# Performance work log

Hardware: AMD Instinct MI355X
Metric: run time of the kernel (lower is better)

Reference implementation:

```python
import jax, jax.numpy as jnp
import numpy as np
from math import sqrt

B, TS_D, SEG, D, H = 16, 2, 1024, 256, 8
D_FF = 1024
DK = D // H
EPS = 1e-5


def _layernorm(x, g, b):
    mu = jnp.mean(x, axis=-1, keepdims=True)
    var = jnp.mean(jnp.square(x - mu), axis=-1, keepdims=True)
    return (x - mu) * jax.lax.rsqrt(var + EPS) * g + b


def setup_inputs() -> dict:
    key = jax.random.key(0)
    ks = jax.random.split(key, 16)
    s = 0.02
    return {
        "x": jax.random.normal(ks[0], (B, TS_D, SEG, D), dtype=jnp.float32),
        "Wq": jax.random.normal(ks[1], (D, D), dtype=jnp.float32) * s,
        "bq": jnp.zeros((D,), jnp.float32),
        "Wk": jax.random.normal(ks[2], (D, D), dtype=jnp.float32) * s,
        "bk": jnp.zeros((D,), jnp.float32),
        "Wv": jax.random.normal(ks[3], (D, D), dtype=jnp.float32) * s,
        "bv": jnp.zeros((D,), jnp.float32),
        "Wo": jax.random.normal(ks[4], (D, D), dtype=jnp.float32) * s,
        "bo": jnp.zeros((D,), jnp.float32),
        "g31": jnp.ones((D,), jnp.float32),
        "b31": jnp.zeros((D,), jnp.float32),
        "W1": jax.random.normal(ks[5], (D, D_FF), dtype=jnp.float32) * s,
        "b1": jnp.zeros((D_FF,), jnp.float32),
        "W2": jax.random.normal(ks[6], (D_FF, D), dtype=jnp.float32) * s,
        "b2": jnp.zeros((D,), jnp.float32),
        "g41": jnp.ones((D,), jnp.float32),
        "b41": jnp.zeros((D,), jnp.float32),
    }


def reference(x, Wq, bq, Wk, bk, Wv, bv, Wo, bo, g31, b31, W1, b1, W2, b2, g41, b41):
    # x: [B, ts_d=2, seg, d]; output is final_out2 (only live path of the module)
    b, ts_d, seg, d = x.shape
    scale = 1.0 / sqrt(DK)
    segments = x.reshape(b, ts_d * seg, d)            # [B, 2*seg, d]
    Q = (segments @ Wq + bq).reshape(b, -1, H, DK)
    K = (segments @ Wk + bk).reshape(b, -1, H, DK)
    V = (segments @ Wv + bv).reshape(b, -1, H, DK)
    q = Q[:, :seg]       # first seg positions (channel 0)
    k = K[:, -seg:]      # last seg positions (channel 1)
    v = V[:, -seg:]
    # cross-segment dual attention
    A1 = jax.nn.softmax(scale * jnp.einsum('blhe,bshe->bhls', q, k), axis=-1)
    out1 = jnp.einsum('bhls,bshd->blhd', A1, v).reshape(b, seg, d)
    A2 = jax.nn.softmax(scale * jnp.einsum('blhe,bshe->bhls', k, q), axis=-1)
    out2 = jnp.einsum('bhls,bshd->blhd', A2, q).reshape(b, seg, d)
    y = jnp.concatenate([out1, out2], axis=1) @ Wo + bo   # [B, 2*seg, d]
    h = _layernorm(segments + y, g31, b31)
    mlp = jax.nn.gelu(h @ W1 + b1, approximate=False) @ W2 + b2
    h = _layernorm(h + mlp, g41, b41)
    return h.reshape(b, ts_d, seg, d)
```

## Files before the change

### kernel.cpp

```cpp
#include <hip/hip_runtime.h>
#include <hip/hip_bf16.h>
#include <math.h>

#define BATCH 16
#define SEG 1024
#define DMODEL 256
#define NH 8
#define DK 32
#define DFF 1024
#define NTOK (BATCH * 2 * SEG)
#define EPS 1e-5f

typedef __attribute__((ext_vector_type(8))) short short8;
typedef __attribute__((ext_vector_type(4))) short short4b;
typedef __attribute__((ext_vector_type(4))) float f32x4;

#if __has_builtin(__builtin_amdgcn_exp2f)
#define EXP2(x) __builtin_amdgcn_exp2f(x)
#else
#define EXP2(x) __expf((x) * 0.6931471805599453f)
#endif

__device__ __forceinline__ ushort f2bf(float x) {
    union { float f; unsigned u; } a; a.f = x;
    unsigned r = a.u + 0x7fffu + ((a.u >> 16) & 1u);
    return (ushort)(r >> 16);
}

typedef const __attribute__((address_space(1))) unsigned gas_u32;
typedef __attribute__((address_space(3))) unsigned las_u32;
__device__ __forceinline__ void gload_lds16(const ushort* g, ushort* l) {
    __builtin_amdgcn_global_load_lds((gas_u32*)g, (las_u32*)l, 16, 0, 0);
}

__global__ __launch_bounds__(256) void wfrag_kernel(
    const float* __restrict__ src, ushort* __restrict__ dst, int K, int N, int order)
{
    const int tid = blockIdx.x * 256 + threadIdx.x;
    const int KT_ = K >> 5, NT_ = N >> 4;
    const int total = KT_ * NT_ * 64;
    if (tid >= total) return;
    const int lane = tid & 63;
    const int frag = tid >> 6;
    int kt, nt;
    if (order) { kt = frag / NT_; nt = frag % NT_; }
    else       { nt = frag / KT_; kt = frag % KT_; }
    const int quad = lane >> 4, l = lane & 15;
    const float* s = src + (size_t)(kt * 32 + quad * 8) * N + nt * 16 + l;
    short8 v;
#pragma unroll
    for (int j = 0; j < 8; j++) v[j] = (short)f2bf(s[(size_t)j * N]);
    *(short8*)&dst[(size_t)tid * 8] = v;
}

#define ASTR 264

__device__ __forceinline__ void dense256_pass(
    const ushort* __restrict__ Wf, ushort* WL, const short8* af,
    f32x4* acc, int t, int w, int lane)
{
#pragma unroll
    for (int nt = 0; nt < 16; ++nt) acc[nt] = (f32x4){0.f, 0.f, 0.f, 0.f};
    {
        const ushort* g = Wf + (size_t)w * 4096 + lane * 8;
        ushort* ld = WL + w * 4096;
#pragma unroll
        for (int i = 0; i < 8; ++i) gload_lds16(g + i * 512, ld + i * 512);
    }
    __syncthreads();
    for (int c = 0; c < 4; ++c) {
        if (c < 3) {
            const ushort* g = Wf + (size_t)(c + 1) * 16384 + w * 4096 + lane * 8;
            ushort* ld = WL + ((c + 1) & 1) * 8192 + w * 4096;
#pragma unroll
            for (int i = 0; i < 8; ++i) gload_lds16(g + i * 512, ld + i * 512);
        }
        const ushort* buf = WL + (c & 1) * 8192;
#pragma unroll
        for (int n2 = 0; n2 < 4; ++n2)
#pragma unroll
            for (int kt = 0; kt < 8; ++kt) {
                const short8 bf_ = *(const short8*)&buf[(n2 * 8 + kt) * 512 + lane * 8];
                acc[c * 4 + n2] = __builtin_amdgcn_mfma_f32_16x16x32_bf16(af[kt], bf_, acc[c * 4 + n2], 0, 0, 0);
            }
        __syncthreads();
    }
}

__global__ __launch_bounds__(256) void qkv_mfma_kernel(
    const float* __restrict__ x,
    const ushort* __restrict__ Wqf, const float* __restrict__ bq,
    const ushort* __restrict__ Wkf, const float* __restrict__ bk,
    const ushort* __restrict__ Wvf, const float* __restrict__ bv,
    ushort* __restrict__ qbuf, ushort* __restrict__ kbuf,
    ushort* __restrict__ qt, ushort* __restrict__ vt)
{
    __shared__ __align__(16) ushort SM[64 * ASTR];
    const int bid = blockIdx.x;
    const int which = bid >> 8;
    const int sub = bid & 255;
    const int b = sub >> 4, ti = sub & 15;
    const int half = (which == 0) ? 0 : 1;
    const int t = threadIdx.x;
    const int w = t >> 6, lane = t & 63, l = lane & 15, quad = lane >> 4;

    const float* xrow = x + ((size_t)b * 2048 + (size_t)half * 1024 + ti * 64) * 256;
#pragma unroll
    for (int p = 0; p < 16; ++p) {
        int ch = t + 256 * p;
        int row = ch >> 6, c4 = ch & 63;
        float4 v = *(const float4*)&xrow[row * 256 + c4 * 4];
        uint2 pk;
        pk.x = (unsigned)f2bf(v.x) | ((unsigned)f2bf(v.y) << 16);
        pk.y = (unsigned)f2bf(v.z) | ((unsigned)f2bf(v.w) << 16);
        *(uint2*)&SM[row * ASTR + c4 * 4] = pk;
    }
    __syncthreads();

    short8 af[8];
#pragma unroll
    for (int kt = 0; kt < 8; ++kt)
        af[kt] = *(const short8*)&SM[(w * 16 + l) * ASTR + kt * 32 + quad * 8];
    __syncthreads();

    const ushort* Wf  = (which == 0) ? Wqf : (which == 1 ? Wkf : Wvf);
    const float* bias = (which == 0) ? bq  : (which == 1 ? bk  : bv);
    const float kscale = (which == 1) ? 0.25503472f : 1.0f;

    f32x4 acc[16];
    dense256_pass(Wf, SM, af, acc, t, w, lane);

    ushort bfv[16][4];
#pragma unroll
    for (int nt = 0; nt < 16; ++nt) {
        const float bb = bias[nt * 16 + l];
#pragma unroll
        for (int r = 0; r < 4; ++r) bfv[nt][r] = f2bf((acc[nt][r] + bb) * kscale);
    }

    if (which <= 1) {
        ushort* obuf = which ? kbuf : qbuf;
#pragma unroll
        for (int nt = 0; nt < 16; ++nt) {
            const int h = nt >> 1, e = (nt & 1) * 16 + l;
#pragma unroll
            for (int r = 0; r < 4; ++r) {
                int tok = ti * 64 + w * 16 + quad * 4 + r;
                obuf[(((size_t)b * 8 + h) * SEG + tok) * 32 + e] = bfv[nt][r];
            }
        }
    }
    if (which != 1) {
        ushort* tb = which ? vt : qt;
#pragma unroll
        for (int nt = 0; nt < 16; ++nt)
#pragma unroll
            for (int r = 0; r < 4; ++r)
                SM[(nt * 16 + l) * 66 + w * 16 + quad * 4 + r] = bfv[nt][r];
        __syncthreads();
        const int d = t, hh = t >> 5, e = t & 31;
        ushort* dr = tb + (((size_t)b * 8 + hh) * 32 + e) * 1024 + ti * 64;
#pragma unroll
        for (int j = 0; j < 8; ++j) {
            uint2 v;
            v.x = *(const unsigned*)&SM[d * 66 + j * 8];
            v.y = *(const unsigned*)&SM[d * 66 + j * 8 + 2];
            unsigned z0 = *(const unsigned*)&SM[d * 66 + j * 8 + 4];
            unsigned z1 = *(const unsigned*)&SM[d * 66 + j * 8 + 6];
            *(uint4*)&dr[j * 8] = make_uint4(v.x, v.y, z0, z1);
        }
    }
}

#define KTILE 128
#define KP 40
#define VP 132

__global__ __launch_bounds__(256) void attn_mfma_kernel(
    const ushort* __restrict__ qbuf, const ushort* __restrict__ kbuf,
    const ushort* __restrict__ qt, const ushort* __restrict__ vt,
    ushort* __restrict__ abuf)
{
    __shared__ __align__(16) ushort Kl[KTILE * KP];
    __shared__ __align__(16) ushort Vl[32 * VP];

    const int bid   = blockIdx.x;
    const int sbh   = bid & 255;
    const int qtile = bid >> 8;
    const int stage = sbh >> 7;
    const int b     = (sbh >> 3) & 15;
    const int h     = sbh & 7;

    const ushort* Qm = stage ? kbuf : qbuf;
    const ushort* Km = stage ? qbuf : kbuf;
    const ushort* Vt = stage ? qt : vt;
    const size_t bh = ((size_t)b * 8 + h) * SEG * 32;

    const int t    = threadIdx.x;
    const int w    = t >> 6;
    const int lane = t & 63;
    const int l    = lane & 15;
    const int quad = lane >> 4;

    const int qrow = qtile * 64 + w * 16 + l;
    const short8 qf = *(const short8*)&Qm[bh + (size_t)qrow * 32 + quad * 8];

    f32x4 o0 = {0.f, 0.f, 0.f, 0.f};
    f32x4 o1 = {0.f, 0.f, 0.f, 0.f};
    f32x4 o2 = {0.f, 0.f, 0.f, 0.f};
    const short4b ones = {(short)0x3F80, (short)0x3F80, (short)0x3F80, (short)0x3F80};

    for (int tile = 0; tile < 8; ++tile) {
        __syncthreads();
        const ushort* Kg = &Km[bh + (size_t)(tile * KTILE) * 32];
#pragma unroll
        for (int p = 0; p < 2; ++p) {
            int ch = t + 256 * p;
            int row = ch >> 2, part = ch & 3;
            *(short8*)&Kl[row * KP + part * 8] = *(const short8*)&Kg[row * 32 + part * 8];
        }
        const ushort* Vg = &Vt[bh + (size_t)tile * KTILE];
#pragma unroll
        for (int p = 0; p < 2; ++p) {
            int ch = t + 256 * p;
            int d = ch >> 4, c = ch & 15;
            *(short8*)&Vl[d * VP + c * 8] = *(const short8*)&Vg[(size_t)d * 1024 + c * 8];
        }
        __syncthreads();

#pragma unroll
        for (int kb = 0; kb < 8; ++kb) {
            const short8 kf = *(const short8*)&Kl[(kb * 16 + l) * KP + quad * 8];
            f32x4 z = {0.f, 0.f, 0.f, 0.f};
            f32x4 sc = __builtin_amdgcn_mfma_f32_16x16x32_bf16(kf, qf, z, 0, 0, 0);
            union { float f; unsigned u; } a0, a1, a2, a3;
            a0.f = EXP2(sc[0]); a1.f = EXP2(sc[1]);
            a2.f = EXP2(sc[2]); a3.f = EXP2(sc[3]);
            unsigned lo = __builtin_amdgcn_perm(a1.u, a0.u, 0x07060302u);
            unsigned hi = __builtin_amdgcn_perm(a3.u, a2.u, 0x07060302u);
            union { uint2 u; short4b s; } pk; pk.u = make_uint2(lo, hi);
            const short4b vf0 = *(const short4b*)&Vl[l * VP + kb * 16 + quad * 4];
            const short4b vf1 = *(const short4b*)&Vl[(16 + l) * VP + kb * 16 + quad * 4];
            o0 = __builtin_amdgcn_mfma_f32_16x16x16bf16_1k(vf0, pk.s, o0, 0, 0, 0);
            o1 = __builtin_amdgcn_mfma_f32_16x16x16bf16_1k(vf1, pk.s, o1, 0, 0, 0);
            o2 = __builtin_amdgcn_mfma_f32_16x16x16bf16_1k(ones, pk.s, o2, 0, 0, 0);
        }
    }

    const float inv = 1.0f / o2[0];
#pragma unroll
    for (int r = 0; r < 4; ++r) { o0[r] *= inv; o1[r] *= inv; }

    __syncthreads();
    ushort* Ob = &Kl[w * 16 * 40];
#pragma unroll
    for (int r = 0; r < 4; ++r) {
        Ob[l * 40 + quad * 4 + r]      = f2bf(o0[r]);
        Ob[l * 40 + 16 + quad * 4 + r] = f2bf(o1[r]);
    }
    __syncthreads();
    const int q = lane >> 2, part = lane & 3;
    const short8 ov = *(const short8*)&Ob[q * 40 + part * 8];
    const int tok = qtile * 64 + w * 16 + q;
    *(short8*)&abuf[((size_t)b * 2 * SEG + (size_t)stage * SEG + tok) * 256 + h * 32 + part * 8] = ov;
}

__global__ __launch_bounds__(256) void proj_mfma_kernel(
    const ushort* __restrict__ abuf, const ushort* __restrict__ Wof,
    const float* __restrict__ bo, const float* __restrict__ x,
    const float* __restrict__ g31, const float* __restrict__ b31,
    float* __restrict__ hout)
{
    __shared__ __align__(16) ushort SM[64 * ASTR];
    const int bid = blockIdx.x;
    const size_t tok0 = (size_t)bid * 64;
    const int t = threadIdx.x;
    const int w = t >> 6, lane = t & 63, l = lane & 15, quad = lane >> 4;

#pragma unroll
    for (int p = 0; p < 8; ++p) {
        int ch = t + 256 * p;
        int row = ch >> 5, c8 = ch & 31;
        *(short8*)&SM[row * ASTR + c8 * 8] = *(const short8*)&abuf[(tok0 + row) * 256 + c8 * 8];
    }
    __syncthreads();

    short8 af[8];
#pragma unroll
    for (int kt = 0; kt < 8; ++kt)
        af[kt] = *(const short8*)&SM[(w * 16 + l) * ASTR + kt * 32 + quad * 8];
    __syncthreads();

    f32x4 acc[16];
    dense256_pass(Wof, SM, af, acc, t, w, lane);

#pragma unroll
    for (int nt = 0; nt < 16; ++nt) {
        const int d = nt * 16 + l;
        const float bv = bo[d];
#pragma unroll
        for (int r = 0; r < 4; ++r) {
            size_t tok = tok0 + w * 16 + quad * 4 + r;
            acc[nt][r] += bv + x[tok * 256 + d];
        }
    }

    float mu_[4], is_[4];
#pragma unroll
    for (int r = 0; r < 4; ++r) {
        float s = 0.f;
#pragma unroll
        for (int nt = 0; nt < 16; ++nt) s += acc[nt][r];
        s += __shfl_xor(s, 1); s += __shfl_xor(s, 2);
        s += __shfl_xor(s, 4); s += __shfl_xor(s, 8);
        float mu = s * (1.0f / 256.0f);
        float vs = 0.f;
#pragma unroll
        for (int nt = 0; nt < 16; ++nt) { float dd = acc[nt][r] - mu; vs += dd * dd; }
        vs += __shfl_xor(vs, 1); vs += __shfl_xor(vs, 2);
        vs += __shfl_xor(vs, 4); vs += __shfl_xor(vs, 8);
        mu_[r] = mu;
        is_[r] = rsqrtf(vs * (1.0f / 256.0f) + EPS);
    }

#pragma unroll
    for (int nt = 0; nt < 16; ++nt) {
        const int d = nt * 16 + l;
        const float gg = g31[d], bb = b31[d];
#pragma unroll
        for (int r = 0; r < 4; ++r) {
            size_t tok = tok0 + w * 16 + quad * 4 + r;
            hout[tok * 256 + d] = (acc[nt][r] - mu_[r]) * is_[r] * gg + bb;
        }
    }
}

#define GP 40

__global__ __launch_bounds__(256) void mlp_mfma_kernel(
    const float* __restrict__ W1dummy_unused, const ushort* __restrict__ W1f,
    const float* __restrict__ b1, const ushort* __restrict__ W2f,
    const float* __restrict__ b2, const float* __restrict__ g41,
    const float* __restrict__ b41, float* __restrict__ io)
{
    __shared__ __align__(16) ushort SM[2 * 16384];
    __shared__ __align__(16) ushort G[4][16 * GP];
    __shared__ __align__(16) float B1L[DFF];
    const int bid = blockIdx.x;
    const size_t tok0 = (size_t)bid * 64;
    const int t = threadIdx.x;
    const int w = t >> 6, lane = t & 63, l = lane & 15, quad = lane >> 4;

    const float* hrow = io + tok0 * 256;
#pragma unroll
    for (int p = 0; p < 16; ++p) {
        int ch = t + 256 * p;
        int row = ch >> 6, c4 = ch & 63;
        float4 v = *(const float4*)&hrow[row * 256 + c4 * 4];
        uint2 pk;
        pk.x = (unsigned)f2bf(v.x) | ((unsigned)f2bf(v.y) << 16);
        pk.y = (unsigned)f2bf(v.z) | ((unsigned)f2bf(v.w) << 16);
        *(uint2*)&SM[row * ASTR + c4 * 4] = pk;
    }
    *(float4*)&B1L[t * 4] = *(const float4*)&b1[t * 4];
    __syncthreads();

    short8 af[8];
#pragma unroll
    for (int kt = 0; kt < 8; ++kt)
        af[kt] = *(const short8*)&SM[(w * 16 + l) * ASTR + kt * 32 + quad * 8];
    __syncthreads();

    f32x4 out[16];
#pragma unroll
    for (int nt = 0; nt < 16; ++nt) out[nt] = (f32x4){0.f, 0.f, 0.f, 0.f};

    ushort* Gw = &G[w][0];

    {
        const ushort* g1 = W1f + w * 2048 + lane * 8;
        const ushort* g2 = W2f + w * 2048 + lane * 8;
        ushort* l1 = SM + w * 2048;
        ushort* l2 = SM + 8192 + w * 2048;
#pragma unroll
        for (int i = 0; i < 4; ++i) {
            gload_lds16(g1 + i * 512, l1 + i * 512);
            gload_lds16(g2 + i * 512, l2 + i * 512);
        }
    }
    __syncthreads();

    for (int c = 0; c < 32; ++c) {
        if (c < 31) {
            const int nb = (c + 1) & 1;
            const ushort* g1 = W1f + (size_t)(c + 1) * 8192 + w * 2048 + lane * 8;
            ushort* l1 = SM + nb * 16384 + w * 2048;
            const ushort* g2 = W2f + (size_t)(c + 1) * 8192 + w * 2048 + lane * 8;
            ushort* l2 = SM + nb * 16384 + 8192 + w * 2048;
#pragma unroll
            for (int i = 0; i < 4; ++i) {
                gload_lds16(g1 + i * 512, l1 + i * 512);
                gload_lds16(g2 + i * 512, l2 + i * 512);
            }
        }
        const ushort* WL = SM + (c & 1) * 16384;

        f32x4 s[2];
        s[0] = (f32x4){0.f, 0.f, 0.f, 0.f};
        s[1] = (f32x4){0.f, 0.f, 0.f, 0.f};
#pragma unroll
        for (int n2 = 0; n2 < 2; ++n2)
#pragma unroll
            for (int kt = 0; kt < 8; ++kt) {
                const short8 bf_ = *(const short8*)&WL[(n2 * 8 + kt) * 512 + lane * 8];
                s[n2] = __builtin_amdgcn_mfma_f32_16x16x32_bf16(af[kt], bf_, s[n2], 0, 0, 0);
            }

#pragma unroll
        for (int n2 = 0; n2 < 2; ++n2) {
            const float bv = B1L[c * 32 + n2 * 16 + l];
#pragma unroll
            for (int r = 0; r < 4; ++r) {
                float v = s[n2][r] + bv;
                float au = fabsf(v) * 0.70710678118654752f;
                float t1 = __builtin_amdgcn_rcpf(fmaf(0.3275911f, au, 1.0f));
                float e  = EXP2(au * au * -1.4426950408889634f);
                float p5 = fmaf(fmaf(fmaf(fmaf(1.061405429f, t1, -1.453152027f),
                                t1, 1.421413741f), t1, -0.284496736f), t1, 0.254829592f) * t1;
                float erf_abs = fmaf(-p5, e, 1.0f);
                float gl = fmaf(0.5f * fabsf(v), erf_abs, 0.5f * v);
                Gw[(quad * 4 + r) * GP + n2 * 16 + l] = f2bf(gl);
            }
        }

        const short8 gf = *(const short8*)&Gw[l * GP + quad * 8];
#pragma unroll
        for (int nt = 0; nt < 16; ++nt) {
            const short8 bf_ = *(const short8*)&WL[8192 + nt * 512 + lane * 8];
            out[nt] = __builtin_amdgcn_mfma_f32_16x16x32_bf16(gf, bf_, out[nt], 0, 0, 0);
        }
        __syncthreads();
    }

#pragma unroll
    for (int nt = 0; nt < 16; ++nt) {
        const int d = nt * 16 + l;
        const float bv = b2[d];
#pragma unroll
        for (int r = 0; r < 4; ++r) {
            size_t tok = tok0 + w * 16 + quad * 4 + r;
            out[nt][r] += bv + io[tok * 256 + d];
        }
    }

    float mu_[4], is_[4];
#pragma unroll
    for (int r = 0; r < 4; ++r) {
        float s = 0.f;
#pragma unroll
        for (int nt = 0; nt < 16; ++nt) s += out[nt][r];
        s += __shfl_xor(s, 1); s += __shfl_xor(s, 2);
        s += __shfl_xor(s, 4); s += __shfl_xor(s, 8);
        float mu = s * (1.0f / 256.0f);
        float vs = 0.f;
#pragma unroll
        for (int nt = 0; nt < 16; ++nt) { float dd = out[nt][r] - mu; vs += dd * dd; }
        vs += __shfl_xor(vs, 1); vs += __shfl_xor(vs, 2);
        vs += __shfl_xor(vs, 4); vs += __shfl_xor(vs, 8);
        mu_[r] = mu;
        is_[r] = rsqrtf(vs * (1.0f / 256.0f) + EPS);
    }

#pragma unroll
    for (int nt = 0; nt < 16; ++nt) {
        const int d = nt * 16 + l;
        const float gg = g41[d], bb = b41[d];
#pragma unroll
        for (int r = 0; r < 4; ++r) {
            size_t tok = tok0 + w * 16 + quad * 4 + r;
            io[tok * 256 + d] = (out[nt][r] - mu_[r]) * is_[r] * gg + bb;
        }
    }
}

extern "C" void kernel_launch(void* const* d_in, const int* in_sizes, int n_in,
                              void* d_out, int out_size, void* d_ws, size_t ws_size,
                              hipStream_t stream)
{
    const float* x   = (const float*)d_in[0];
    const float* Wq  = (const float*)d_in[1];
    const float* bq  = (const float*)d_in[2];
    const float* Wk  = (const float*)d_in[3];
    const float* bk  = (const float*)d_in[4];
    const float* Wv  = (const float*)d_in[5];
    const float* bv  = (const float*)d_in[6];
    const float* Wo  = (const float*)d_in[7];
    const float* bo  = (const float*)d_in[8];
    const float* g31 = (const float*)d_in[9];
    const float* b31 = (const float*)d_in[10];
    const float* W1  = (const float*)d_in[11];
    const float* b1  = (const float*)d_in[12];
    const float* W2  = (const float*)d_in[13];
    const float* b2  = (const float*)d_in[14];
    const float* g41 = (const float*)d_in[15];
    const float* b41 = (const float*)d_in[16];

    float* out = (float*)d_out;

    const size_t HALF = (size_t)BATCH * SEG * DMODEL;
    ushort* qbuf = (ushort*)d_ws;
    ushort* kbuf = qbuf + HALF;
    ushort* qt   = kbuf + HALF;
    ushort* vt   = qt + HALF;
    ushort* abuf = vt + HALF;
    ushort* Wqf  = abuf + 2 * HALF;
    ushort* Wkf  = Wqf + 65536;
    ushort* Wvf  = Wkf + 65536;
    ushort* Wof  = Wvf + 65536;
    ushort* W1f  = Wof + 65536;
    ushort* W2f  = W1f + 262144;

    wfrag_kernel<<<32, 256, 0, stream>>>(Wq, Wqf, 256, 256, 0);
    wfrag_kernel<<<32, 256, 0, stream>>>(Wk, Wkf, 256, 256, 0);
    wfrag_kernel<<<32, 256, 0, stream>>>(Wv, Wvf, 256, 256, 0);
    wfrag_kernel<<<32, 256, 0, stream>>>(Wo, Wof, 256, 256, 0);
    wfrag_kernel<<<128, 256, 0, stream>>>(W1, W1f, 256, 1024, 0);
    wfrag_kernel<<<128, 256, 0, stream>>>(W2, W2f, 1024, 256, 1);

    qkv_mfma_kernel<<<768, 256, 0, stream>>>(x, Wqf, bq, Wkf, bk, Wvf, bv,
                                             qbuf, kbuf, qt, vt);
    attn_mfma_kernel<<<2 * BATCH * NH * (SEG / 64), 256, 0, stream>>>(qbuf, kbuf, qt, vt, abuf);
    proj_mfma_kernel<<<NTOK / 64, 256, 0, stream>>>(abuf, Wof, bo, x, g31, b31, out);
    mlp_mfma_kernel<<<NTOK / 64, 256, 0, stream>>>(nullptr, W1f, b1, W2f, b2, g41, b41, out);
}
```

Before: 284.9 us.

## Fuse projection and MLP kernels, batch weight conversion, prefetch K/V tiles

Merges the six weight-fragment conversion launches into one kernel that picks its matrix by block index. Fuses the output-projection plus LayerNorm kernel into the MLP kernel, so h stays in registers and LDS as bf16 instead of going through global memory in fp32. The attention kernel now register-prefetches the next K/V tile while the current one is computed, with a different K row mapping. The fused kernel keeps more live registers (acc plus out), and the __launch_bounds__(256,2) hint may force register spilling.

```diff
diff --git a/kernel.cpp b/kernel.cpp
--- a/kernel.cpp
+++ b/kernel.cpp
@@ -33,13 +33,24 @@
     __builtin_amdgcn_global_load_lds((gas_u32*)g, (las_u32*)l, 16, 0, 0);
 }
 
-__global__ __launch_bounds__(256) void wfrag_kernel(
-    const float* __restrict__ src, ushort* __restrict__ dst, int K, int N, int order)
+__global__ __launch_bounds__(256) void wfrag_all_kernel(
+    const float* __restrict__ Wq, const float* __restrict__ Wk,
+    const float* __restrict__ Wv, const float* __restrict__ Wo,
+    const float* __restrict__ W1, const float* __restrict__ W2,
+    ushort* __restrict__ Wqf, ushort* __restrict__ Wkf,
+    ushort* __restrict__ Wvf, ushort* __restrict__ Wof,
+    ushort* __restrict__ W1f, ushort* __restrict__ W2f)
 {
-    const int tid = blockIdx.x * 256 + threadIdx.x;
+    const int blk = blockIdx.x;
+    const float* src; ushort* dst; int K, N, order, base;
+    if (blk < 32)       { src = Wq; dst = Wqf; K = 256;  N = 256;  order = 0; base = 0;   }
+    else if (blk < 64)  { src = Wk; dst = Wkf; K = 256;  N = 256;  order = 0; base = 32;  }
+    else if (blk < 96)  { src = Wv; dst = Wvf; K = 256;  N = 256;  order = 0; base = 64;  }
+    else if (blk < 128) { src = Wo; dst = Wof; K = 256;  N = 256;  order = 0; base = 96;  }
+    else if (blk < 256) { src = W1; dst = W1f; K = 256;  N = 1024; order = 0; base = 128; }
+    else                { src = W2; dst = W2f; K = 1024; N = 256;  order = 1; base = 256; }
+    const int tid = (blk - base) * 256 + threadIdx.x;
     const int KT_ = K >> 5, NT_ = N >> 4;
-    const int total = KT_ * NT_ * 64;
-    if (tid >= total) return;
     const int lane = tid & 63;
     const int frag = tid >> 6;
     int kt, nt;
@@ -210,23 +221,35 @@
     f32x4 o2 = {0.f, 0.f, 0.f, 0.f};
     const short4b ones = {(short)0x3F80, (short)0x3F80, (short)0x3F80, (short)0x3F80};
 
+    const int ch0 = t, ch1 = t + 256;
+    const int kr0 = ((ch0 >> 6) << 4) | (ch0 & 15), kp0 = (ch0 >> 4) & 3;
+    const int kr1 = ((ch1 >> 6) << 4) | (ch1 & 15), kp1 = (ch1 >> 4) & 3;
+    const int vd0 = ch0 >> 4, vc0 = ch0 & 15;
+    const int vd1 = ch1 >> 4, vc1 = ch1 & 15;
+    const ushort* Kgb = &Km[bh];
+    const ushort* Vgb = &Vt[bh];
+
+    short8 rk0 = *(const short8*)&Kgb[(size_t)kr0 * 32 + kp0 * 8];
+    short8 rk1 = *(const short8*)&Kgb[(size_t)kr1 * 32 + kp1 * 8];
+    short8 rv0 = *(const short8*)&Vgb[(size_t)vd0 * 1024 + vc0 * 8];
+    short8 rv1 = *(const short8*)&Vgb[(size_t)vd1 * 1024 + vc1 * 8];
+
     for (int tile = 0; tile < 8; ++tile) {
         __syncthreads();
-        const ushort* Kg = &Km[bh + (size_t)(tile * KTILE) * 32];
-#pragma unroll
-        for (int p = 0; p < 2; ++p) {
-            int ch = t + 256 * p;
-            int row = ch >> 2, part = ch & 3;
-            *(short8*)&Kl[row * KP + part * 8] = *(const short8*)&Kg[row * 32 + part * 8];
-        }
-        const ushort* Vg = &Vt[bh + (size_t)tile * KTILE];
-#pragma unroll
-        for (int p = 0; p < 2; ++p) {
-            int ch = t + 256 * p;
-            int d = ch >> 4, c = ch & 15;
-            *(short8*)&Vl[d * VP + c * 8] = *(const short8*)&Vg[(size_t)d * 1024 + c * 8];
-        }
+        *(short8*)&Kl[kr0 * KP + kp0 * 8] = rk0;
+        *(short8*)&Kl[kr1 * KP + kp1 * 8] = rk1;
+        *(short8*)&Vl[vd0 * VP + vc0 * 8] = rv0;
+        *(short8*)&Vl[vd1 * VP + vc1 * 8] = rv1;
         __syncthreads();
+
+        if (tile < 7) {
+            const size_t ko = (size_t)(tile + 1) * KTILE * 32;
+            const size_t vo = (size_t)(tile + 1) * KTILE;
+            rk0 = *(const short8*)&Kgb[ko + (size_t)kr0 * 32 + kp0 * 8];
+            rk1 = *(const short8*)&Kgb[ko + (size_t)kr1 * 32 + kp1 * 8];
+            rv0 = *(const short8*)&Vgb[vo + (size_t)vd0 * 1024 + vc0 * 8];
+            rv1 = *(const short8*)&Vgb[vo + (size_t)vd1 * 1024 + vc1 * 8];
+        }
 
 #pragma unroll
         for (int kb = 0; kb < 8; ++kb) {
@@ -265,83 +288,16 @@
     *(short8*)&abuf[((size_t)b * 2 * SEG + (size_t)stage * SEG + tok) * 256 + h * 32 + part * 8] = ov;
 }
 
-__global__ __launch_bounds__(256) void proj_mfma_kernel(
+#define GP 40
+
+__global__ __launch_bounds__(256, 2) void proj_mlp_kernel(
     const ushort* __restrict__ abuf, const ushort* __restrict__ Wof,
     const float* __restrict__ bo, const float* __restrict__ x,
     const float* __restrict__ g31, const float* __restrict__ b31,
-    float* __restrict__ hout)
-{
-    __shared__ __align__(16) ushort SM[64 * ASTR];
-    const int bid = blockIdx.x;
-    const size_t tok0 = (size_t)bid * 64;
-    const int t = threadIdx.x;
-    const int w = t >> 6, lane = t & 63, l = lane & 15, quad = lane >> 4;
-
-#pragma unroll
-    for (int p = 0; p < 8; ++p) {
-        int ch = t + 256 * p;
-        int row = ch >> 5, c8 = ch & 31;
-        *(short8*)&SM[row * ASTR + c8 * 8] = *(const short8*)&abuf[(tok0 + row) * 256 + c8 * 8];
-    }
-    __syncthreads();
-
-    short8 af[8];
-#pragma unroll
-    for (int kt = 0; kt < 8; ++kt)
-        af[kt] = *(const short8*)&SM[(w * 16 + l) * ASTR + kt * 32 + quad * 8];
-    __syncthreads();
-
-    f32x4 acc[16];
-    dense256_pass(Wof, SM, af, acc, t, w, lane);
-
-#pragma unroll
-    for (int nt = 0; nt < 16; ++nt) {
-        const int d = nt * 16 + l;
-        const float bv = bo[d];
-#pragma unroll
-        for (int r = 0; r < 4; ++r) {
-            size_t tok = tok0 + w * 16 + quad * 4 + r;
-            acc[nt][r] += bv + x[tok * 256 + d];
-        }
-    }
-
-    float mu_[4], is_[4];
-#pragma unroll
-    for (int r = 0; r < 4; ++r) {
-        float s = 0.f;
-#pragma unroll
-        for (int nt = 0; nt < 16; ++nt) s += acc[nt][r];
-        s += __shfl_xor(s, 1); s += __shfl_xor(s, 2);
-        s += __shfl_xor(s, 4); s += __shfl_xor(s, 8);
-        float mu = s * (1.0f / 256.0f);
-        float vs = 0.f;
-#pragma unroll
-        for (int nt = 0; nt < 16; ++nt) { float dd = acc[nt][r] - mu; vs += dd * dd; }
-        vs += __shfl_xor(vs, 1); vs += __shfl_xor(vs, 2);
-        vs += __shfl_xor(vs, 4); vs += __shfl_xor(vs, 8);
-        mu_[r] = mu;
-        is_[r] = rsqrtf(vs * (1.0f / 256.0f) + EPS);
-    }
-
-#pragma unroll
-    for (int nt = 0; nt < 16; ++nt) {
-        const int d = nt * 16 + l;
-        const float gg = g31[d], bb = b31[d];
-#pragma unroll
-        for (int r = 0; r < 4; ++r) {
-            size_t tok = tok0 + w * 16 + quad * 4 + r;
-            hout[tok * 256 + d] = (acc[nt][r] - mu_[r]) * is_[r] * gg + bb;
-        }
-    }
-}
-
-#define GP 40
-
-__global__ __launch_bounds__(256) void mlp_mfma_kernel(
-    const float* __restrict__ W1dummy_unused, const ushort* __restrict__ W1f,
-    const float* __restrict__ b1, const ushort* __restrict__ W2f,
-    const float* __restrict__ b2, const float* __restrict__ g41,
-    const float* __restrict__ b41, float* __restrict__ io)
+    const ushort* __restrict__ W1f, const float* __restrict__ b1,
+    const ushort* __restrict__ W2f, const float* __restrict__ b2,
+    const float* __restrict__ g41, const float* __restrict__ b41,
+    float* __restrict__ io)
 {
     __shared__ __align__(16) ushort SM[2 * 16384];
     __shared__ __align__(16) ushort G[4][16 * GP];
@@ -351,21 +307,65 @@
     const int t = threadIdx.x;
     const int w = t >> 6, lane = t & 63, l = lane & 15, quad = lane >> 4;
 
-    const float* hrow = io + tok0 * 256;
-#pragma unroll
-    for (int p = 0; p < 16; ++p) {
+#pragma unroll
+    for (int p = 0; p < 8; ++p) {
         int ch = t + 256 * p;
-        int row = ch >> 6, c4 = ch & 63;
-        float4 v = *(const float4*)&hrow[row * 256 + c4 * 4];
-        uint2 pk;
-        pk.x = (unsigned)f2bf(v.x) | ((unsigned)f2bf(v.y) << 16);
-        pk.y = (unsigned)f2bf(v.z) | ((unsigned)f2bf(v.w) << 16);
-        *(uint2*)&SM[row * ASTR + c4 * 4] = pk;
+        int row = ch >> 5, c8 = ch & 31;
+        *(short8*)&SM[row * ASTR + c8 * 8] = *(const short8*)&abuf[(tok0 + row) * 256 + c8 * 8];
     }
     *(float4*)&B1L[t * 4] = *(const float4*)&b1[t * 4];
     __syncthreads();
 
     short8 af[8];
+#pragma unroll
+    for (int kt = 0; kt < 8; ++kt)
+        af[kt] = *(const short8*)&SM[(w * 16 + l) * ASTR + kt * 32 + quad * 8];
+    __syncthreads();
+
+    f32x4 acc[16];
+    dense256_pass(Wof, SM, af, acc, t, w, lane);
+
+#pragma unroll
+    for (int nt = 0; nt < 16; ++nt) {
+        const int d = nt * 16 + l;
+        const float bv = bo[d];
+#pragma unroll
+        for (int r = 0; r < 4; ++r) {
+            size_t tok = tok0 + w * 16 + quad * 4 + r;
+            acc[nt][r] += bv + x[tok * 256 + d];
+        }
+    }
+    {
+        float mu_[4], is_[4];
+#pragma unroll
+        for (int r = 0; r < 4; ++r) {
+            float s = 0.f;
+#pragma unroll
+            for (int nt = 0; nt < 16; ++nt) s += acc[nt][r];
+            s += __shfl_xor(s, 1); s += __shfl_xor(s, 2);
+            s += __shfl_xor(s, 4); s += __shfl_xor(s, 8);
+            float mu = s * (1.0f / 256.0f);
+            float vs = 0.f;
+#pragma unroll
+            for (int nt = 0; nt < 16; ++nt) { float dd = acc[nt][r] - mu; vs += dd * dd; }
+            vs += __shfl_xor(vs, 1); vs += __shfl_xor(vs, 2);
+            vs += __shfl_xor(vs, 4); vs += __shfl_xor(vs, 8);
+            mu_[r] = mu;
+            is_[r] = rsqrtf(vs * (1.0f / 256.0f) + EPS);
+        }
+#pragma unroll
+        for (int nt = 0; nt < 16; ++nt) {
+            const int d = nt * 16 + l;
+            const float gg = g31[d], bb = b31[d];
+#pragma unroll
+            for (int r = 0; r < 4; ++r) {
+                float hv = (acc[nt][r] - mu_[r]) * is_[r] * gg + bb;
+                acc[nt][r] = hv;
+                SM[(w * 16 + quad * 4 + r) * ASTR + d] = f2bf(hv);
+            }
+        }
+    }
+    __syncthreads();
 #pragma unroll
     for (int kt = 0; kt < 8; ++kt)
         af[kt] = *(const short8*)&SM[(w * 16 + l) * ASTR + kt * 32 + quad * 8];
@@ -405,23 +405,22 @@
         }
         const ushort* WL = SM + (c & 1) * 16384;
 
-        f32x4 s[2];
-        s[0] = (f32x4){0.f, 0.f, 0.f, 0.f};
-        s[1] = (f32x4){0.f, 0.f, 0.f, 0.f};
-#pragma unroll
-        for (int n2 = 0; n2 < 2; ++n2)
-#pragma unroll
-            for (int kt = 0; kt < 8; ++kt) {
-                const short8 bf_ = *(const short8*)&WL[(n2 * 8 + kt) * 512 + lane * 8];
-                s[n2] = __builtin_amdgcn_mfma_f32_16x16x32_bf16(af[kt], bf_, s[n2], 0, 0, 0);
-            }
+        f32x4 s0 = {0.f, 0.f, 0.f, 0.f};
+        f32x4 s1 = {0.f, 0.f, 0.f, 0.f};
+#pragma unroll
+        for (int kt = 0; kt < 8; ++kt) {
+            const short8 b0 = *(const short8*)&WL[kt * 512 + lane * 8];
+            const short8 b1_ = *(const short8*)&WL[(8 + kt) * 512 + lane * 8];
+            s0 = __builtin_amdgcn_mfma_f32_16x16x32_bf16(af[kt], b0, s0, 0, 0, 0);
+            s1 = __builtin_amdgcn_mfma_f32_16x16x32_bf16(af[kt], b1_, s1, 0, 0, 0);
+        }
 
 #pragma unroll
         for (int n2 = 0; n2 < 2; ++n2) {
             const float bv = B1L[c * 32 + n2 * 16 + l];
 #pragma unroll
             for (int r = 0; r < 4; ++r) {
-                float v = s[n2][r] + bv;
+                float v = (n2 ? s1[r] : s0[r]) + bv;
                 float au = fabsf(v) * 0.70710678118654752f;
                 float t1 = __builtin_amdgcn_rcpf(fmaf(0.3275911f, au, 1.0f));
                 float e  = EXP2(au * au * -1.4426950408889634f);
@@ -447,10 +446,8 @@
         const int d = nt * 16 + l;
         const float bv = b2[d];
 #pragma unroll
-        for (int r = 0; r < 4; ++r) {
-            size_t tok = tok0 + w * 16 + quad * 4 + r;
-            out[nt][r] += bv + io[tok * 256 + d];
-        }
+        for (int r = 0; r < 4; ++r)
+            out[nt][r] += bv + acc[nt][r];
     }
 
     float mu_[4], is_[4];
@@ -520,16 +517,12 @@
     ushort* W1f  = Wof + 65536;
     ushort* W2f  = W1f + 262144;
 
-    wfrag_kernel<<<32, 256, 0, stream>>>(Wq, Wqf, 256, 256, 0);
-    wfrag_kernel<<<32, 256, 0, stream>>>(Wk, Wkf, 256, 256, 0);
-    wfrag_kernel<<<32, 256, 0, stream>>>(Wv, Wvf, 256, 256, 0);
-    wfrag_kernel<<<32, 256, 0, stream>>>(Wo, Wof, 256, 256, 0);
-    wfrag_kernel<<<128, 256, 0, stream>>>(W1, W1f, 256, 1024, 0);
-    wfrag_kernel<<<128, 256, 0, stream>>>(W2, W2f, 1024, 256, 1);
+    wfrag_all_kernel<<<384, 256, 0, stream>>>(Wq, Wk, Wv, Wo, W1, W2,
+                                              Wqf, Wkf, Wvf, Wof, W1f, W2f);
 
     qkv_mfma_kernel<<<768, 256, 0, stream>>>(x, Wqf, bq, Wkf, bk, Wvf, bv,
                                              qbuf, kbuf, qt, vt);
     attn_mfma_kernel<<<2 * BATCH * NH * (SEG / 64), 256, 0, stream>>>(qbuf, kbuf, qt, vt, abuf);
-    proj_mfma_kernel<<<NTOK / 64, 256, 0, stream>>>(abuf, Wof, bo, x, g31, b31, out);
-    mlp_mfma_kernel<<<NTOK / 64, 256, 0, stream>>>(nullptr, W1f, b1, W2f, b2, g41, b41, out);
-}
+    proj_mlp_kernel<<<NTOK / 64, 256, 0, stream>>>(abuf, Wof, bo, x, g31, b31,
+                                                   W1f, b1, W2f, b2, g41, b41, out);
+}
```

After: 266.1 us (median of 2 runs). 6.6% less time.
